# Optimization experiments

Measured on AMD Instinct MI355X. Metric: run time of the kernel, lower is better.

## Reference

```python
import jax, jax.numpy as jnp
import numpy as np

DIM = 256
HEADS = 8
HEAD_DIM = DIM // HEADS
WS = 8           # window_size
TOPK = 4
BN_EPS = 1e-5


def _window_partition(x, ws):
    b, c, h, w = x.shape
    pad_h = (ws - h % ws) % ws
    pad_w = (ws - w % ws) % ws
    x = jnp.pad(x, ((0, 0), (0, 0), (0, pad_h), (0, pad_w)))
    hp, wp = x.shape[-2:]
    x = x.reshape(b, c, hp // ws, ws, wp // ws, ws)
    x = jnp.transpose(x, (0, 2, 4, 3, 5, 1)).reshape(b, -1, ws * ws, c)
    return x, (hp, wp)


def _window_reverse(windows, padded_hw, original_hw, ws):
    b, num_windows, tokens, c = windows.shape
    hp, wp = padded_hw
    x = windows.reshape(b, hp // ws, wp // ws, ws, ws, c)
    x = jnp.transpose(x, (0, 5, 1, 3, 2, 4)).reshape(b, c, hp, wp)
    h, w = original_hw
    return x[:, :, :h, :w]


def setup_inputs() -> dict:
    key = jax.random.key(0)
    ks = jax.random.split(key, 9)
    b, c, h, w = 8, DIM, 64, 64
    s = 1.0 / np.sqrt(c)
    return {
        "x": jax.random.normal(ks[0], (b, c, h, w), jnp.float32),
        "prompt": jax.random.normal(ks[1], (b, c, h, w), jnp.float32),
        "Wq": jax.random.normal(ks[2], (c, c), jnp.float32) * s,
        "Wk": jax.random.normal(ks[3], (c, c), jnp.float32) * s,
        "Wv": jax.random.normal(ks[4], (c, c), jnp.float32) * s,
        "Wproj": jax.random.normal(ks[5], (c, c), jnp.float32) * s,
        "Wg": jax.random.normal(ks[6], (c, 2 * c), jnp.float32) * (1.0 / np.sqrt(2 * c)),
        "bn_gamma": jnp.ones((c,), jnp.float32),
        "bn_beta": jnp.zeros((c,), jnp.float32),
    }


def reference(x, prompt, Wq, Wk, Wv, Wproj, Wg, bn_gamma, bn_beta):
    b, c, h, w = x.shape
    x_windows, padded_hw = _window_partition(x, WS)        # [b, nwx, T, c]
    p_windows, _ = _window_partition(prompt, WS)           # [b, nwp, T, c]
    T = WS * WS

    # --- routing: window descriptors -> topk prompt windows per query window
    x_desc = x_windows.mean(axis=2)                        # [b, nwx, c]
    p_desc = p_windows.mean(axis=2)                        # [b, nwp, c]
    score = jnp.einsum("bqc,bkc->bqk", x_desc, p_desc) / jnp.sqrt(jnp.float32(c))
    topk = min(TOPK, p_windows.shape[1])
    routed = jax.lax.top_k(score, topk)[1]                 # [b, nwx, topk]

    # --- gather routed kv windows (vmapped per-batch gather)
    selected = jax.vmap(lambda pw, idx: pw[idx])(p_windows, routed)  # [b, nwx, topk, T, c]
    nwx = x_windows.shape[1]
    kv = selected.reshape(b, nwx, topk * T, c)

    # --- windowed cross-attention (float32 internally, like the torch module)
    def heads_split(t):
        return jnp.transpose(
            t.reshape(t.shape[0], t.shape[1], t.shape[2], HEADS, HEAD_DIM),
            (0, 1, 3, 2, 4))                                # [b, nw, H, L, hd]

    q = heads_split(jnp.einsum("bnqc,oc->bnqo", x_windows, Wq).astype(jnp.float32))
    k = heads_split(jnp.einsum("bnkc,oc->bnko", kv, Wk).astype(jnp.float32))
    v = heads_split(jnp.einsum("bnkc,oc->bnko", kv, Wv).astype(jnp.float32))

    attn = jnp.einsum("bnhqd,bnhkd->bnhqk", q, k) * (HEAD_DIM ** -0.5)
    attn = jax.nn.softmax(attn, axis=-1)
    out = jnp.einsum("bnhqk,bnhkd->bnhqd", attn, v)
    out = jnp.transpose(out, (0, 1, 3, 2, 4)).reshape(b, nwx, T, c).astype(x.dtype)
    y_windows = jnp.einsum("bnqc,oc->bnqo", out, Wproj)

    y = _window_reverse(y_windows, padded_hw, (h, w), WS)  # [b, c, h, w]

    # --- gate: 1x1 conv -> BatchNorm2d (training-mode batch stats) -> sigmoid
    cat = jnp.concatenate([x, y], axis=1)                  # [b, 2c, h, w]
    g = jnp.einsum("bihw,oi->bohw", cat, Wg)
    mean = g.mean(axis=(0, 2, 3), keepdims=True)
    var = g.var(axis=(0, 2, 3), keepdims=True)             # biased, as torch BN
    g = (g - mean) * jax.lax.rsqrt(var + BN_EPS)
    g = g * bn_gamma[None, :, None, None] + bn_beta[None, :, None, None]
    gate = jax.nn.sigmoid(g)

    return x + gate * y
```

## Files before the change

kernel.cpp:

```cpp
#include <hip/hip_runtime.h>
#include <math.h>

#define B 8
#define Cc 256
#define P 4096
#define NW 64
#define NH 8
#define HD 32
#define TOPK 4
#define SCALE 0.17677669529663687f
#define EXP2S 0.2550348640579426f

typedef unsigned short u16;
typedef __attribute__((ext_vector_type(4))) float f32x4;
typedef __attribute__((ext_vector_type(8))) short s16x8;
typedef __attribute__((ext_vector_type(4))) unsigned short u16x4;

#define MFMA(a, b, c) __builtin_amdgcn_mfma_f32_16x16x32_bf16(a, b, c, 0, 0, 0)

__device__ inline u16 f2bf(float f) {
  unsigned u = __float_as_uint(f);
  return (u16)((u + 0x7fffu + ((u >> 16) & 1u)) >> 16);
}
__device__ inline float bf2f(u16 h) { return __uint_as_float(((unsigned)h) << 16); }

__global__ __launch_bounds__(256) void pack_kernel(
    const float* __restrict__ x, const float* __restrict__ prompt,
    const float* __restrict__ Wq, const float* __restrict__ Wk,
    const float* __restrict__ Wv, const float* __restrict__ Wproj,
    const float* __restrict__ Wg,
    u16* __restrict__ XY, u16* __restrict__ PT, float* __restrict__ Pd,
    u16* __restrict__ Wbf) {
  if (blockIdx.z == 4) {
    int id = blockIdx.y * 64 + blockIdx.x;
    if (id >= 640) return;
    int job = id >> 7;
    const float* src;
    u16* dst;
    int n;
    switch (job) {
      case 0: src = Wq;    dst = Wbf;          n = 65536;  break;
      case 1: src = Wk;    dst = Wbf + 65536;  n = 65536;  break;
      case 2: src = Wv;    dst = Wbf + 131072; n = 65536;  break;
      case 3: src = Wproj; dst = Wbf + 196608; n = 65536;  break;
      default: src = Wg;   dst = Wbf + 262144; n = 131072; break;
    }
    int i = ((id & 127) * 256 + threadIdx.x) * 4;
    if (i < n) {
      float4 v = *(const float4*)(src + i);
      u16x4 o = {f2bf(v.x), f2bf(v.y), f2bf(v.z), f2bf(v.w)};
      *(u16x4*)(dst + i) = o;
    }
    return;
  }
  __shared__ u16 ldsd[64 * 68];
  __shared__ float pdl[64 * 9];
  int y = blockIdx.x;
  int sb = blockIdx.y;
  int cq = blockIdx.z;
  int sel = sb >> 3, b = sb & 7;
  const float* src =
      (sel ? prompt : x) + (size_t)(b * 256 + cq * 64) * 4096 + y * 64;
  int tid = threadIdx.x;
  int pxg = tid & 15;
  int cr = tid >> 4;
  int px0 = pxg * 4;
#pragma unroll
  for (int iter = 0; iter < 4; ++iter) {
    int cl = iter * 16 + cr;
    float4 v = *(const float4*)(src + (size_t)cl * 4096 + px0);
    u16x4 o = {f2bf(v.x), f2bf(v.y), f2bf(v.z), f2bf(v.w)};
    int sw = ((cl >> 3) & 3) << 2;
    *(u16x4*)(ldsd + cl * 68 + (px0 ^ sw)) = o;
    float s4 = (v.x + v.y) + (v.z + v.w);
    float s8 = s4 + __shfl_xor(s4, 1);
    if ((pxg & 1) == 0) pdl[cl * 9 + (pxg >> 1)] = s8;
  }
  __syncthreads();
  int tok = tid >> 2, cg = tid & 3;
  int n = ((y >> 3) << 3) + (tok >> 3);
  int tk = ((y & 7) << 3) + (tok & 7);
  size_t prow = (size_t)b * 4096 + n * 64 + tk;
  u16* dst = (sel ? (PT + prow * 256) : (XY + prow * 512)) + cq * 64;
#pragma unroll
  for (int cc = 0; cc < 2; ++cc) {
    int cb = cg * 8 + cc * 32;
    s16x8 v;
#pragma unroll
    for (int j = 0; j < 8; ++j) {
      int cl = cb + j;
      int sw = ((cl >> 3) & 3) << 2;
      v[j] = (short)ldsd[cl * 68 + (tok ^ sw)];
    }
    *(s16x8*)(dst + cb) = v;
  }
  float* pd = Pd + ((size_t)sb * 64 + y) * 2048 + cq * 64;
#pragma unroll
  for (int i = 0; i < 2; ++i) {
    int e = i * 256 + tid;
    int wx = e >> 6, cl = e & 63;
    pd[wx * 256 + cl] = pdl[cl * 9 + wx];
  }
}

__global__ __launch_bounds__(256) void dred_kernel(
    const float* __restrict__ Pd, float* __restrict__ dx, float* __restrict__ dp) {
  int sb = blockIdx.x;
  int sel = sb >> 3, b = sb & 7;
  int c = threadIdx.x;
  float* dst = (sel ? dp : dx) + ((size_t)b * 256 + c) * 64;
  const float* src = Pd + (size_t)sb * 64 * 2048;
#pragma unroll
  for (int nn = 0; nn < 8; ++nn) {
    int n = blockIdx.y * 8 + nn;
    int wy = n >> 3, wx = n & 7;
    float s = 0.f;
#pragma unroll
    for (int yl = 0; yl < 8; ++yl)
      s += src[((wy * 8 + yl) * 8 + wx) * 256 + c];
    dst[n] = s * (1.f / 64.f);
  }
}

__global__ __launch_bounds__(64) void route_kernel(
    const float* __restrict__ dx, const float* __restrict__ dp,
    int* __restrict__ routed) {
  int bq = blockIdx.x;
  int b = bq >> 6;
  int q = bq & 63;
  int lane = threadIdx.x;
  const float* dxb = dx + (size_t)b * Cc * NW;
  const float* dpb = dp + (size_t)b * Cc * NW;
  float s = 0.f;
  for (int c = 0; c < Cc; ++c)
    s = fmaf(dxb[c * NW + q], dpb[c * NW + lane], s);
  s *= (1.f / 16.f);
  for (int kk = 0; kk < TOPK; ++kk) {
    float v = s;
    int i = lane;
    for (int off = 32; off; off >>= 1) {
      float ov = __shfl_xor(v, off);
      int oi = __shfl_xor(i, off);
      if (ov > v || (ov == v && oi < i)) { v = ov; i = oi; }
    }
    if (lane == 0) routed[bq * TOPK + kk] = i;
    if (lane == i) s = -INFINITY;
  }
}

__device__ __forceinline__ void gemm_core(
    const u16* __restrict__ A, int lda, const u16* __restrict__ W, int K,
    int m0, int n0, int tid, u16* Asm, u16* Wsm, f32x4 (&acc)[4][4]) {
  int l = tid & 63, wv = tid >> 6;
  int lq = l & 15, g = l >> 4;
  int wm = (wv & 1) * 64, wn = (wv >> 1) * 64;
  for (int k0 = 0; k0 < K; k0 += 64) {
    s16x8 av[4], wvv[4];
#pragma unroll
    for (int i = 0; i < 4; ++i) {
      int s = i * 256 + tid, row = s >> 3, u = s & 7;
      av[i] = *(const s16x8*)(A + (size_t)(m0 + row) * lda + k0 + u * 8);
      wvv[i] = *(const s16x8*)(W + (size_t)(n0 + row) * K + k0 + u * 8);
    }
    __syncthreads();
#pragma unroll
    for (int i = 0; i < 4; ++i) {
      int s = i * 256 + tid, row = s >> 3, u = s & 7;
      int gu = u ^ (row & 7);
      *(s16x8*)(Asm + row * 64 + gu * 8) = av[i];
      *(s16x8*)(Wsm + row * 64 + gu * 8) = wvv[i];
    }
    __syncthreads();
#pragma unroll
    for (int ks = 0; ks < 2; ++ks) {
      s16x8 af[4], bfr[4];
#pragma unroll
      for (int mi = 0; mi < 4; ++mi) {
        int r = wm + 16 * mi + lq;
        af[mi] = *(const s16x8*)(Asm + r * 64 + ((4 * ks + g) ^ (r & 7)) * 8);
      }
#pragma unroll
      for (int ni = 0; ni < 4; ++ni) {
        int r = wn + 16 * ni + lq;
        bfr[ni] = *(const s16x8*)(Wsm + r * 64 + ((4 * ks + g) ^ (r & 7)) * 8);
      }
#pragma unroll
      for (int mi = 0; mi < 4; ++mi)
#pragma unroll
        for (int ni = 0; ni < 4; ++ni)
          acc[mi][ni] = MFMA(af[mi], bfr[ni], acc[mi][ni]);
    }
  }
}

__device__ __forceinline__ void store_rowmajor(
    f32x4 (&acc)[4][4], u16* __restrict__ Out, int ldo,
    size_t mbase, int nbase, int lq, int g) {
#pragma unroll
  for (int mi = 0; mi < 4; ++mi) {
    size_t mrow = mbase + 16 * mi + 4 * g;
#pragma unroll
    for (int r = 0; r < 4; ++r) {
      u16* orow = Out + (mrow + r) * ldo + nbase + lq;
#pragma unroll
      for (int ni = 0; ni < 4; ++ni)
        orow[16 * ni] = f2bf(acc[mi][ni][r]);
    }
  }
}

__device__ __forceinline__ void store_chanmajor(
    f32x4 (&acc)[4][4], u16* __restrict__ Out,
    int bb, int tb, int cbase, int lq) {
#pragma unroll
  for (int ni = 0; ni < 4; ++ni) {
    u16* ocol = Out + ((size_t)(bb * 256) + cbase + 16 * ni + lq) * 4096 + tb;
#pragma unroll
    for (int mi = 0; mi < 4; ++mi) {
      u16x4 pk = {f2bf(acc[mi][ni][0]), f2bf(acc[mi][ni][1]),
                  f2bf(acc[mi][ni][2]), f2bf(acc[mi][ni][3])};
      *(u16x4*)(ocol + 16 * mi) = pk;
    }
  }
}

__global__ __launch_bounds__(256) void qkv_kernel(
    const u16* __restrict__ XY, const u16* __restrict__ PT,
    const u16* __restrict__ Wbf, u16* __restrict__ QT,
    u16* __restrict__ KT, u16* __restrict__ VT) {
  __shared__ u16 Asm[8192], Wsm[8192];
  int jy = blockIdx.y, m0 = blockIdx.x * 128;
  int tid = threadIdx.x;
  int l = tid & 63, wv = tid >> 6;
  int lq = l & 15, g = l >> 4;
  int wm = (wv & 1) * 64, wn = (wv >> 1) * 64;
  f32x4 acc[4][4];
#pragma unroll
  for (int mi = 0; mi < 4; ++mi)
#pragma unroll
    for (int ni = 0; ni < 4; ++ni)
      acc[mi][ni] = (f32x4){0.f, 0.f, 0.f, 0.f};

  const u16* A;
  const u16* W;
  int lda, n0;
  if (jy < 2) { A = XY; lda = 512; W = Wbf; n0 = jy * 128; }
  else        { A = PT; lda = 256; W = Wbf + 65536; n0 = (jy - 2) * 128; }
  gemm_core(A, lda, W, 256, m0, n0, tid, Asm, Wsm, acc);

  if (jy < 2) {
    store_rowmajor(acc, QT, 256, (size_t)(m0 + wm), n0 + wn, lq, g);
  } else if (n0 < 256) {
    store_rowmajor(acc, KT, 256, (size_t)(m0 + wm), n0 + wn, lq, g);
  } else {
    store_chanmajor(acc, VT, m0 >> 12, (m0 & 4095) + wm + 4 * g,
                    (n0 - 256) + wn, lq);
  }
}

__global__ __launch_bounds__(256) void gate_kernel(
    const u16* __restrict__ XY, const u16* __restrict__ Wbf,
    u16* __restrict__ GT, float* __restrict__ pS, float* __restrict__ pSS) {
  __shared__ u16 Asm[8192], Wsm[8192];
  int m0 = blockIdx.x * 128, n0 = blockIdx.y * 128;
  int tid = threadIdx.x;
  int l = tid & 63, wv = tid >> 6;
  int lq = l & 15, g = l >> 4;
  int wm = (wv & 1) * 64, wn = (wv >> 1) * 64;
  f32x4 acc[4][4];
#pragma unroll
  for (int mi = 0; mi < 4; ++mi)
#pragma unroll
    for (int ni = 0; ni < 4; ++ni)
      acc[mi][ni] = (f32x4){0.f, 0.f, 0.f, 0.f};
  gemm_core(XY, 512, Wbf + 262144, 512, m0, n0, tid, Asm, Wsm, acc);
  store_rowmajor(acc, GT, 256, (size_t)(m0 + wm), n0 + wn, lq, g);

  float cs[4], cq[4];
#pragma unroll
  for (int ni = 0; ni < 4; ++ni) {
    float s = 0.f, q2 = 0.f;
#pragma unroll
    for (int mi = 0; mi < 4; ++mi)
#pragma unroll
      for (int r = 0; r < 4; ++r) {
        float v = acc[mi][ni][r];
        s += v;
        q2 = fmaf(v, v, q2);
      }
    cs[ni] = s;
    cq[ni] = q2;
  }
#pragma unroll
  for (int ni = 0; ni < 4; ++ni) {
    cs[ni] += __shfl_xor(cs[ni], 16);
    cs[ni] += __shfl_xor(cs[ni], 32);
    cq[ni] += __shfl_xor(cq[ni], 16);
    cq[ni] += __shfl_xor(cq[ni], 32);
  }
  float* sS = (float*)Asm;
  float* sQ = sS + 128;
  __syncthreads();
  if ((wv & 1) == 0 && g == 0) {
#pragma unroll
    for (int ni = 0; ni < 4; ++ni) {
      int col = wn + 16 * ni + lq;
      sS[col] = cs[ni];
      sQ[col] = cq[ni];
    }
  }
  __syncthreads();
  if ((wv & 1) == 1 && g == 0) {
#pragma unroll
    for (int ni = 0; ni < 4; ++ni) {
      int col = wn + 16 * ni + lq;
      sS[col] += cs[ni];
      sQ[col] += cq[ni];
    }
  }
  __syncthreads();
  if (tid < 128) {
    pS[(size_t)blockIdx.x * 256 + n0 + tid] = sS[tid];
    pSS[(size_t)blockIdx.x * 256 + n0 + tid] = sQ[tid];
  }
}

__global__ __launch_bounds__(512) void attn_kernel(
    const u16* __restrict__ Qb, const u16* __restrict__ Kb,
    const u16* __restrict__ Vt, const int* __restrict__ routed,
    const u16* __restrict__ Wp, u16* __restrict__ XY) {
  __shared__ char Plds[40960];
  int bn = blockIdx.x, b = bn >> 6, n = bn & 63;
  int h = threadIdx.x >> 6, l = threadIdx.x & 63;
  int lq = l & 15, g = l >> 4;
  char* Pw = Plds + h * 5120;

  const u16* Qrow = Qb + ((size_t)(b * 4096) + n * 64) * 256 + h * 32 + g * 8;
  s16x8 qf[4];
#pragma unroll
  for (int qi = 0; qi < 4; ++qi)
    qf[qi] = *(const s16x8*)(Qrow + (16 * qi + lq) * 256);

  f32x4 acc[4][2];
#pragma unroll
  for (int qi = 0; qi < 4; ++qi) {
    acc[qi][0] = (f32x4){0.f, 0.f, 0.f, 0.f};
    acc[qi][1] = (f32x4){0.f, 0.f, 0.f, 0.f};
  }
  float denom[4] = {0.f, 0.f, 0.f, 0.f};
  const f32x4 zero4 = {0.f, 0.f, 0.f, 0.f};
  const int* rptr = routed + bn * TOPK;

  for (int kk = 0; kk < TOPK; ++kk) {
    int pw = __builtin_amdgcn_readfirstlane(rptr[kk]);
    const u16* Krow = Kb + ((size_t)(b * 4096) + pw * 64) * 256 + h * 32 + g * 8;
    const u16* Vrow = Vt + ((size_t)(b * 256) + h * 32 + lq) * 4096 + pw * 64 + 8 * g;
#pragma unroll
    for (int half = 0; half < 2; ++half) {
#pragma unroll
      for (int kvil = 0; kvil < 2; ++kvil) {
        int kvi = half * 2 + kvil;
        s16x8 kf = *(const s16x8*)(Krow + (16 * kvi + lq) * 256);
        f32x4 sv[4];
#pragma unroll
        for (int qi = 0; qi < 4; ++qi)
          sv[qi] = MFMA(kf, qf[qi], zero4);
#pragma unroll
        for (int qi = 0; qi < 4; ++qi) {
          float p0 = __builtin_amdgcn_exp2f(sv[qi][0] * EXP2S);
          float p1 = __builtin_amdgcn_exp2f(sv[qi][1] * EXP2S);
          float p2 = __builtin_amdgcn_exp2f(sv[qi][2] * EXP2S);
          float p3 = __builtin_amdgcn_exp2f(sv[qi][3] * EXP2S);
          denom[qi] += (p0 + p1) + (p2 + p3);
          uint2 pk;
          pk.x = (unsigned)f2bf(p0) | ((unsigned)f2bf(p1) << 16);
          pk.y = (unsigned)f2bf(p2) | ((unsigned)f2bf(p3) << 16);
          int q = 16 * qi + lq;
          *(uint2*)(Pw + q * 80 + (16 * kvil + 4 * g) * 2) = pk;
        }
      }
      s16x8 vf[2];
#pragma unroll
      for (int di = 0; di < 2; ++di)
        vf[di] = *(const s16x8*)(Vrow + (size_t)(16 * di) * 4096 + 32 * half);
#pragma unroll
      for (int qi = 0; qi < 4; ++qi) {
        int q = 16 * qi + lq;
        s16x8 pf = *(const s16x8*)(Pw + q * 80 + 16 * g);
#pragma unroll
        for (int di = 0; di < 2; ++di)
          acc[qi][di] = MFMA(pf, vf[di], acc[qi][di]);
      }
    }
  }

#pragma unroll
  for (int qi = 0; qi < 4; ++qi) {
    denom[qi] += __shfl_xor(denom[qi], 16);
    denom[qi] += __shfl_xor(denom[qi], 32);
  }

  __syncthreads();
  char* Ot = Plds;
#pragma unroll
  for (int qi = 0; qi < 4; ++qi) {
    float inv = 1.f / denom[qi];
#pragma unroll
    for (int r = 0; r < 4; ++r) {
      float nr = __shfl(inv, 4 * g + r);
      int t = 16 * qi + 4 * g + r;
      char* rowp = Ot + t * 512;
#pragma unroll
      for (int di = 0; di < 2; ++di) {
        int c = h * 32 + 16 * di + lq;
        *(u16*)(rowp + ((c * 2) ^ ((t & 7) << 4))) =
            f2bf(acc[qi][di][r] * nr);
      }
    }
  }
  __syncthreads();

  f32x4 acc2[4][2];
#pragma unroll
  for (int mi = 0; mi < 4; ++mi) {
    acc2[mi][0] = (f32x4){0.f, 0.f, 0.f, 0.f};
    acc2[mi][1] = (f32x4){0.f, 0.f, 0.f, 0.f};
  }
#pragma unroll
  for (int k0 = 0; k0 < 256; k0 += 32) {
    s16x8 af[4], bfr[2];
#pragma unroll
    for (int mi = 0; mi < 4; ++mi) {
      int t = 16 * mi + lq;
      af[mi] = *(const s16x8*)(Ot + t * 512 +
                               (((k0 + 8 * g) * 2) ^ ((t & 7) << 4)));
    }
#pragma unroll
    for (int ni = 0; ni < 2; ++ni)
      bfr[ni] = *(const s16x8*)(Wp + (size_t)(h * 32 + 16 * ni + lq) * 256 +
                                k0 + 8 * g);
#pragma unroll
    for (int mi = 0; mi < 4; ++mi)
#pragma unroll
      for (int ni = 0; ni < 2; ++ni)
        acc2[mi][ni] = MFMA(af[mi], bfr[ni], acc2[mi][ni]);
  }

  u16* Yrow = XY + ((size_t)(b * 4096) + n * 64) * 512 + 256 + h * 32;
#pragma unroll
  for (int mi = 0; mi < 4; ++mi)
#pragma unroll
    for (int r = 0; r < 4; ++r) {
      u16* orow = Yrow + (size_t)(16 * mi + 4 * g + r) * 512 + lq;
#pragma unroll
      for (int ni = 0; ni < 2; ++ni)
        orow[16 * ni] = f2bf(acc2[mi][ni][r]);
    }
}

__global__ __launch_bounds__(1024) void bnfin_kernel(
    const float* __restrict__ pS, const float* __restrict__ pSS,
    const float* __restrict__ gamma, const float* __restrict__ beta,
    float* __restrict__ scale, float* __restrict__ shift) {
  int tid = threadIdx.x;
  int c = tid >> 2, part = tid & 3;
  float S = 0.f, SS = 0.f;
  for (int m = part * 64; m < part * 64 + 64; ++m) {
    S += pS[m * 256 + c];
    SS += pSS[m * 256 + c];
  }
  __shared__ float rS[4][256], rQ[4][256];
  rS[part][c] = S;
  rQ[part][c] = SS;
  __syncthreads();
  if (tid < 256) {
    int cc = tid;
    float S2 = rS[0][cc] + rS[1][cc] + rS[2][cc] + rS[3][cc];
    float Q2 = rQ[0][cc] + rQ[1][cc] + rQ[2][cc] + rQ[3][cc];
    const float invN = 1.f / 32768.f;
    float mean = S2 * invN;
    float var = Q2 * invN - mean * mean;
    float sc = rsqrtf(var + 1e-5f) * gamma[cc];
    scale[cc] = sc;
    shift[cc] = beta[cc] - mean * sc;
  }
}

__global__ __launch_bounds__(256) void final_kernel(
    const float* __restrict__ x, const u16* __restrict__ XY,
    const u16* __restrict__ GT, const float* __restrict__ scale,
    const float* __restrict__ shift, float* __restrict__ out) {
  __shared__ u16 Yl[64 * 256];
  __shared__ u16 Gl[64 * 256];
  __shared__ float sSc[256], sSh[256];
  int y = blockIdx.x, b = blockIdx.y;
  int tid = threadIdx.x;
  sSc[tid] = scale[tid];
  sSh[tid] = shift[tid];
  {
    int r = tid >> 2;
    int n = ((y >> 3) << 3) + (r >> 3);
    int t = ((y & 7) << 3) + (r & 7);
    size_t prow = (size_t)b * 4096 + n * 64 + t;
    const u16* ysrc = XY + prow * 512 + 256;
    const u16* gsrc = GT + prow * 256;
#pragma unroll
    for (int cc = 0; cc < 8; ++cc) {
      int chunk = (tid & 3) * 8 + cc;
      int off = r * 256 + ((chunk ^ (r & 31)) << 3);
      *(s16x8*)(Yl + off) = *(const s16x8*)(ysrc + chunk * 8);
      *(s16x8*)(Gl + off) = *(const s16x8*)(gsrc + chunk * 8);
    }
  }
  __syncthreads();
  int lane = tid & 63, wq = tid >> 6;
  size_t base = (size_t)(b * 256) * 4096 + y * 64 + lane;
#pragma unroll 2
  for (int ch = 0; ch < 8; ++ch) {
    int chunk = wq * 8 + ch;
    int off = lane * 256 + ((chunk ^ (lane & 31)) << 3);
    s16x8 yv = *(const s16x8*)(Yl + off);
    s16x8 gv = *(const s16x8*)(Gl + off);
#pragma unroll
    for (int j = 0; j < 8; ++j) {
      int c = chunk * 8 + j;
      size_t a = base + (size_t)c * 4096;
      float gate = 1.f / (1.f + __expf(-fmaf(bf2f((u16)gv[j]), sSc[c], sSh[c])));
      out[a] = x[a] + gate * bf2f((u16)yv[j]);
    }
  }
}

extern "C" void kernel_launch(void* const* d_in, const int* in_sizes, int n_in,
                              void* d_out, int out_size, void* d_ws, size_t ws_size,
                              hipStream_t stream) {
  const float* x      = (const float*)d_in[0];
  const float* prompt = (const float*)d_in[1];
  const float* Wq     = (const float*)d_in[2];
  const float* Wk     = (const float*)d_in[3];
  const float* Wv     = (const float*)d_in[4];
  const float* Wproj  = (const float*)d_in[5];
  const float* Wg     = (const float*)d_in[6];
  const float* gamma  = (const float*)d_in[7];
  const float* beta   = (const float*)d_in[8];

  char* wsb = (char*)d_ws;
  u16* XY    = (u16*)(wsb + 0);
  u16* PT    = (u16*)(wsb + 33554432);
  u16* QT    = (u16*)(wsb + 50331648);
  u16* KT    = (u16*)(wsb + 67108864);
  u16* VT    = (u16*)(wsb + 83886080);
  u16* Wbf   = (u16*)(wsb + 117440512);
  float* dx  = (float*)(wsb + 118226944);
  float* dp  = (float*)(wsb + 118751232);
  float* scl = (float*)(wsb + 119275520);
  float* shf = (float*)(wsb + 119276544);
  int* routed = (int*)(wsb + 119277568);
  float* Pd  = (float*)QT;
  float* pS  = (float*)KT;
  float* pSS = (float*)(wsb + 67108864 + 262144);
  u16* GT = QT;

  pack_kernel<<<dim3(64, 16, 5), 256, 0, stream>>>(
      x, prompt, Wq, Wk, Wv, Wproj, Wg, XY, PT, Pd, Wbf);
  dred_kernel<<<dim3(16, 8), 256, 0, stream>>>(Pd, dx, dp);
  route_kernel<<<B * NW, 64, 0, stream>>>(dx, dp, routed);
  qkv_kernel<<<dim3(256, 6), 256, 0, stream>>>(XY, PT, Wbf, QT, KT, VT);
  attn_kernel<<<B * NW, 512, 0, stream>>>(QT, KT, VT, routed,
                                          Wbf + 196608, XY);
  gate_kernel<<<dim3(256, 2), 256, 0, stream>>>(XY, Wbf, GT, pS, pSS);
  bnfin_kernel<<<1, 1024, 0, stream>>>(pS, pSS, gamma, beta, scl, shf);
  final_kernel<<<dim3(64, 8), 256, 0, stream>>>(x, XY, GT, scl, shf, (float*)d_out);
}
```

Baseline: 158.5 us.

## Split attention KV windows across two wave groups per block with LDS reduction

The attention kernel now launches 1024 threads per block. Each head gets two waves, and each wave processes two of the four routed KV windows. Partial unnormalized outputs and denominators from the second half go through LDS and are added into the first half before normalization. The output projection is then split so each wave computes 16 of its head's 32 output columns. This raises parallelism for the 512-block grid, at the cost of doubled LDS (80KB), extra syncs, and an fp32 reduction pass.

```diff
diff --git a/kernel.cpp b/kernel.cpp
--- a/kernel.cpp
+++ b/kernel.cpp
@@ -325,15 +325,17 @@
   }
 }
 
-__global__ __launch_bounds__(512) void attn_kernel(
+__global__ __launch_bounds__(1024, 8) void attn_kernel(
     const u16* __restrict__ Qb, const u16* __restrict__ Kb,
     const u16* __restrict__ Vt, const int* __restrict__ routed,
     const u16* __restrict__ Wp, u16* __restrict__ XY) {
-  __shared__ char Plds[40960];
+  __shared__ char Plds[81920];
   int bn = blockIdx.x, b = bn >> 6, n = bn & 63;
-  int h = threadIdx.x >> 6, l = threadIdx.x & 63;
+  int wid = threadIdx.x >> 6;
+  int h = wid & 7, half = wid >> 3;
+  int l = threadIdx.x & 63;
   int lq = l & 15, g = l >> 4;
-  char* Pw = Plds + h * 5120;
+  char* Pw = Plds + wid * 5120;
 
   const u16* Qrow = Qb + ((size_t)(b * 4096) + n * 64) * 256 + h * 32 + g * 8;
   s16x8 qf[4];
@@ -351,15 +353,16 @@
   const f32x4 zero4 = {0.f, 0.f, 0.f, 0.f};
   const int* rptr = routed + bn * TOPK;
 
-  for (int kk = 0; kk < TOPK; ++kk) {
-    int pw = __builtin_amdgcn_readfirstlane(rptr[kk]);
+#pragma unroll
+  for (int kx = 0; kx < 2; ++kx) {
+    int pw = __builtin_amdgcn_readfirstlane(rptr[half * 2 + kx]);
     const u16* Krow = Kb + ((size_t)(b * 4096) + pw * 64) * 256 + h * 32 + g * 8;
     const u16* Vrow = Vt + ((size_t)(b * 256) + h * 32 + lq) * 4096 + pw * 64 + 8 * g;
 #pragma unroll
-    for (int half = 0; half < 2; ++half) {
+    for (int hh = 0; hh < 2; ++hh) {
 #pragma unroll
       for (int kvil = 0; kvil < 2; ++kvil) {
-        int kvi = half * 2 + kvil;
+        int kvi = hh * 2 + kvil;
         s16x8 kf = *(const s16x8*)(Krow + (16 * kvi + lq) * 256);
         f32x4 sv[4];
 #pragma unroll
@@ -382,7 +385,7 @@
       s16x8 vf[2];
 #pragma unroll
       for (int di = 0; di < 2; ++di)
-        vf[di] = *(const s16x8*)(Vrow + (size_t)(16 * di) * 4096 + 32 * half);
+        vf[di] = *(const s16x8*)(Vrow + (size_t)(16 * di) * 4096 + 32 * hh);
 #pragma unroll
       for (int qi = 0; qi < 4; ++qi) {
         int q = 16 * qi + lq;
@@ -401,61 +404,88 @@
   }
 
   __syncthreads();
+  float* Of = (float*)Plds;
+  float* db = (float*)(Plds + 66560);
+  if (half == 1) {
+#pragma unroll
+    for (int qi = 0; qi < 4; ++qi)
+#pragma unroll
+      for (int r = 0; r < 4; ++r) {
+        int t = 16 * qi + 4 * g + r;
+#pragma unroll
+        for (int di = 0; di < 2; ++di)
+          Of[t * 260 + h * 32 + 16 * di + lq] = acc[qi][di][r];
+      }
+    if (g == 0) {
+#pragma unroll
+      for (int qi = 0; qi < 4; ++qi)
+        db[h * 64 + 16 * qi + lq] = denom[qi];
+    }
+  }
+  __syncthreads();
+  if (half == 0) {
+#pragma unroll
+    for (int qi = 0; qi < 4; ++qi)
+      denom[qi] += db[h * 64 + 16 * qi + lq];
+#pragma unroll
+    for (int qi = 0; qi < 4; ++qi)
+#pragma unroll
+      for (int r = 0; r < 4; ++r) {
+        int t = 16 * qi + 4 * g + r;
+#pragma unroll
+        for (int di = 0; di < 2; ++di)
+          acc[qi][di][r] += Of[t * 260 + h * 32 + 16 * di + lq];
+      }
+  }
+  __syncthreads();
+
   char* Ot = Plds;
-#pragma unroll
-  for (int qi = 0; qi < 4; ++qi) {
-    float inv = 1.f / denom[qi];
-#pragma unroll
-    for (int r = 0; r < 4; ++r) {
-      float nr = __shfl(inv, 4 * g + r);
-      int t = 16 * qi + 4 * g + r;
-      char* rowp = Ot + t * 512;
-#pragma unroll
-      for (int di = 0; di < 2; ++di) {
-        int c = h * 32 + 16 * di + lq;
-        *(u16*)(rowp + ((c * 2) ^ ((t & 7) << 4))) =
-            f2bf(acc[qi][di][r] * nr);
-      }
-    }
-  }
-  __syncthreads();
-
-  f32x4 acc2[4][2];
-#pragma unroll
-  for (int mi = 0; mi < 4; ++mi) {
-    acc2[mi][0] = (f32x4){0.f, 0.f, 0.f, 0.f};
-    acc2[mi][1] = (f32x4){0.f, 0.f, 0.f, 0.f};
-  }
+  if (half == 0) {
+#pragma unroll
+    for (int qi = 0; qi < 4; ++qi) {
+      float inv = 1.f / denom[qi];
+#pragma unroll
+      for (int r = 0; r < 4; ++r) {
+        float nr = __shfl(inv, 4 * g + r);
+        int t = 16 * qi + 4 * g + r;
+        char* rowp = Ot + t * 512;
+#pragma unroll
+        for (int di = 0; di < 2; ++di) {
+          int c = h * 32 + 16 * di + lq;
+          *(u16*)(rowp + ((c * 2) ^ ((t & 7) << 4))) =
+              f2bf(acc[qi][di][r] * nr);
+        }
+      }
+    }
+  }
+  __syncthreads();
+
+  int cb = h * 32 + half * 16;
+  f32x4 acc2[4];
+#pragma unroll
+  for (int mi = 0; mi < 4; ++mi)
+    acc2[mi] = (f32x4){0.f, 0.f, 0.f, 0.f};
 #pragma unroll
   for (int k0 = 0; k0 < 256; k0 += 32) {
-    s16x8 af[4], bfr[2];
+    s16x8 af[4];
 #pragma unroll
     for (int mi = 0; mi < 4; ++mi) {
       int t = 16 * mi + lq;
       af[mi] = *(const s16x8*)(Ot + t * 512 +
                                (((k0 + 8 * g) * 2) ^ ((t & 7) << 4)));
     }
-#pragma unroll
-    for (int ni = 0; ni < 2; ++ni)
-      bfr[ni] = *(const s16x8*)(Wp + (size_t)(h * 32 + 16 * ni + lq) * 256 +
-                                k0 + 8 * g);
+    s16x8 bfr = *(const s16x8*)(Wp + (size_t)(cb + lq) * 256 + k0 + 8 * g);
 #pragma unroll
     for (int mi = 0; mi < 4; ++mi)
-#pragma unroll
-      for (int ni = 0; ni < 2; ++ni)
-        acc2[mi][ni] = MFMA(af[mi], bfr[ni], acc2[mi][ni]);
-  }
-
-  u16* Yrow = XY + ((size_t)(b * 4096) + n * 64) * 512 + 256 + h * 32;
+      acc2[mi] = MFMA(af[mi], bfr, acc2[mi]);
+  }
+
+  u16* Yrow = XY + ((size_t)(b * 4096) + n * 64) * 512 + 256 + cb;
 #pragma unroll
   for (int mi = 0; mi < 4; ++mi)
 #pragma unroll
-    for (int r = 0; r < 4; ++r) {
-      u16* orow = Yrow + (size_t)(16 * mi + 4 * g + r) * 512 + lq;
-#pragma unroll
-      for (int ni = 0; ni < 2; ++ni)
-        orow[16 * ni] = f2bf(acc2[mi][ni][r]);
-    }
+    for (int r = 0; r < 4; ++r)
+      Yrow[(size_t)(16 * mi + 4 * g + r) * 512 + lq] = f2bf(acc2[mi][r]);
 }
 
 __global__ __launch_bounds__(1024) void bnfin_kernel(
@@ -566,8 +596,8 @@
   dred_kernel<<<dim3(16, 8), 256, 0, stream>>>(Pd, dx, dp);
   route_kernel<<<B * NW, 64, 0, stream>>>(dx, dp, routed);
   qkv_kernel<<<dim3(256, 6), 256, 0, stream>>>(XY, PT, Wbf, QT, KT, VT);
-  attn_kernel<<<B * NW, 512, 0, stream>>>(QT, KT, VT, routed,
-                                          Wbf + 196608, XY);
+  attn_kernel<<<B * NW, 1024, 0, stream>>>(QT, KT, VT, routed,
+                                           Wbf + 196608, XY);
   gate_kernel<<<dim3(256, 2), 256, 0, stream>>>(XY, Wbf, GT, pS, pSS);
   bnfin_kernel<<<1, 1024, 0, stream>>>(pS, pSS, gamma, beta, scl, shf);
   final_kernel<<<dim3(64, 8), 256, 0, stream>>>(x, XY, GT, scl, shf, (float*)d_out);
```

Result: slower. 313.4 us (+97.8%).
